# Kernel tuning notes

Hardware: AMD Instinct MI355X
Metric: run time of the kernel (lower is better)

The kernel has to match this reference:

```python
import jax, jax.numpy as jnp
import numpy as np

N_HEADS = 4
DIM_HEAD = 32


def setup_inputs() -> dict:
    key = jax.random.key(0)
    k1, k2, k3, k4 = jax.random.split(key, 4)
    x = jax.random.normal(k1, (8, 64, 80, 1024), dtype=jnp.float32)
    # conv_qkv: 1x1 conv, no bias -> weight [3*heads*dim_head, dim_in_out]
    w_qkv = jax.random.normal(k2, (3 * N_HEADS * DIM_HEAD, 64), dtype=jnp.float32) * 0.05
    # conv_out: 1x1 conv with bias -> weight [dim_in_out, heads*dim_head], bias [dim_in_out]
    w_out = jax.random.normal(k3, (64, N_HEADS * DIM_HEAD), dtype=jnp.float32) * 0.05
    b_out = jax.random.normal(k4, (64,), dtype=jnp.float32) * 0.05
    return {"x": x, "w_qkv": w_qkv, "w_out": w_out, "b_out": b_out}


def reference(x, w_qkv, w_out, b_out):
    b, c, h, w = x.shape
    n = h * w
    # 1x1 conv == channel matmul
    qkv = jnp.einsum('bchw,oc->bohw', x, w_qkv)            # [b, 3*heads*dh, h, w]
    qkv = qkv.reshape(b, 3, N_HEADS, DIM_HEAD, n)          # qkv outermost, then heads, then c
    q, k, v = qkv[:, 0], qkv[:, 1], qkv[:, 2]              # each [b, heads, dh, n]
    k = jax.nn.softmax(k, axis=-1)                          # softmax over spatial positions
    context = jnp.einsum('bhdn,bhen->bhde', k, v)          # [b, heads, dh, dh]
    out = jnp.einsum('bhde,bhdn->bhen', context, q)        # [b, heads, dh, n]
    out = out.reshape(b, N_HEADS * DIM_HEAD, h, w)
    return jnp.einsum('bchw,oc->bohw', out, w_out) + b_out[None, :, None, None]
```

## Files before the change

kernel.cpp:

```cpp
#include <hip/hip_runtime.h>
#include <stdint.h>


#define N_POS 81920
#define NT    128
#define TILES 640

typedef short bf16x8 __attribute__((ext_vector_type(8)));
typedef float f32x4  __attribute__((ext_vector_type(4)));

__device__ __forceinline__ uint32_t packbf(float lo, float hi){
  uint32_t a = __float_as_uint(lo), b = __float_as_uint(hi);
  a = (a + 0x8000u) >> 16;
  b = (b + 0x8000u) & 0xffff0000u;
  return a | b;
}
__device__ __forceinline__ short bf16of(float v){
  return (short)((__float_as_uint(v) + 0x8000u) >> 16);
}

__global__ __launch_bounds__(512, 4) void kernA(
    const float* __restrict__ x, const float* __restrict__ w,
    float* __restrict__ pA, float* __restrict__ pZ, int nch, int tpc)
{
  __shared__ __align__(16) uint16_t xs_cp[64 * 136];
  __shared__ __align__(16) uint16_t xs_pc[128 * 72];
  __shared__ __align__(16) uint16_t es[128 * 136];

  const int t  = threadIdx.x;
  const int w8 = t >> 6;
  const int l  = t & 63;
  const int lm = l & 15;
  const int lg = l >> 4;

  const int b  = blockIdx.x / nch;
  const int ch = blockIdx.x % nch;
  const float* xb = x + (size_t)b * 64 * N_POS;

  const int rr  = t >> 3;
  const int pg  = t & 7;
  const int spp = t & 127;
  const int scg = t >> 7;

  const int pth = w8 & 3;
  const int ht0 = (w8 >> 2) * 4;

  bf16x8 wkf[4][2];
  #pragma unroll
  for (int i = 0; i < 4; ++i)
    #pragma unroll
    for (int kk = 0; kk < 2; ++kk){
      const float* wp = w + (size_t)(128 + 16*(ht0+i) + lm) * 64 + 32*kk + 8*lg;
      float4 w0 = *(const float4*)wp;
      float4 w1 = *(const float4*)(wp + 4);
      bf16x8 f;
      f[0]=bf16of(w0.x); f[1]=bf16of(w0.y); f[2]=bf16of(w0.z); f[3]=bf16of(w0.w);
      f[4]=bf16of(w1.x); f[5]=bf16of(w1.y); f[6]=bf16of(w1.z); f[7]=bf16of(w1.w);
      wkf[i][kk] = f;
    }

  bf16x8 ones;
  #pragma unroll
  for (int j = 0; j < 8; ++j) ones[j] = (short)0x3F80;

  f32x4 acc[4], zac;
  zac = (f32x4){0.f,0.f,0.f,0.f};
  #pragma unroll
  for (int n = 0; n < 4; ++n) acc[n] = (f32x4){0.f,0.f,0.f,0.f};

  float4 fa0, fa1, fa2, fa3;
  float v[16];
  {
    const int n0 = (ch * tpc) * NT;
    const float* ga = xb + (size_t)rr * N_POS + n0 + 16*pg;
    fa0 = *(const float4*)ga;       fa1 = *(const float4*)(ga + 4);
    fa2 = *(const float4*)(ga + 8); fa3 = *(const float4*)(ga + 12);
    const float* gb = xb + (size_t)(16*scg) * N_POS + n0 + spp;
    #pragma unroll
    for (int i = 0; i < 16; ++i) v[i] = gb[(size_t)i * N_POS];
  }

  for (int tile = 0; tile < tpc; ++tile){
    __syncthreads();
    {
      uint4 u0, u1;
      u0.x = packbf(fa0.x,fa0.y); u0.y = packbf(fa0.z,fa0.w);
      u0.z = packbf(fa1.x,fa1.y); u0.w = packbf(fa1.z,fa1.w);
      u1.x = packbf(fa2.x,fa2.y); u1.y = packbf(fa2.z,fa2.w);
      u1.z = packbf(fa3.x,fa3.y); u1.w = packbf(fa3.z,fa3.w);
      *(uint4*)&xs_cp[rr*136 + 16*pg]     = u0;
      *(uint4*)&xs_cp[rr*136 + 16*pg + 8] = u1;
      uint4 p0, p1;
      p0.x = packbf(v[0],v[1]);   p0.y = packbf(v[2],v[3]);
      p0.z = packbf(v[4],v[5]);   p0.w = packbf(v[6],v[7]);
      p1.x = packbf(v[8],v[9]);   p1.y = packbf(v[10],v[11]);
      p1.z = packbf(v[12],v[13]); p1.w = packbf(v[14],v[15]);
      *(uint4*)&xs_pc[spp*72 + 16*scg]     = p0;
      *(uint4*)&xs_pc[spp*72 + 16*scg + 8] = p1;
    }
    __syncthreads();
    if (tile + 1 < tpc){
      const int n1 = (ch * tpc + tile + 1) * NT;
      const float* ga = xb + (size_t)rr * N_POS + n1 + 16*pg;
      fa0 = *(const float4*)ga;       fa1 = *(const float4*)(ga + 4);
      fa2 = *(const float4*)(ga + 8); fa3 = *(const float4*)(ga + 12);
      const float* gb = xb + (size_t)(16*scg) * N_POS + n1 + spp;
      #pragma unroll
      for (int i = 0; i < 16; ++i) v[i] = gb[(size_t)i * N_POS];
    }
    #pragma unroll
    for (int ip = 0; ip < 2; ++ip){
      const int pt = pth + 4*ip;
      bf16x8 af0 = *(const bf16x8*)&xs_pc[(16*pt + lm)*72 + 8*lg];
      bf16x8 af1 = *(const bf16x8*)&xs_pc[(16*pt + lm)*72 + 32 + 8*lg];
      #pragma unroll
      for (int i = 0; i < 4; ++i){
        f32x4 s = (f32x4){0.f,0.f,0.f,0.f};
        s = __builtin_amdgcn_mfma_f32_16x16x32_bf16(af0, wkf[i][0], s, 0,0,0);
        s = __builtin_amdgcn_mfma_f32_16x16x32_bf16(af1, wkf[i][1], s, 0,0,0);
        float e0 = __expf(s[0]), e1 = __expf(s[1]);
        float e2 = __expf(s[2]), e3 = __expf(s[3]);
        uint2 pk; pk.x = packbf(e0,e1); pk.y = packbf(e2,e3);
        *(uint2*)&es[(16*(ht0+i) + lm)*136 + 16*pt + 4*lg] = pk;
      }
    }
    __syncthreads();
    __builtin_amdgcn_s_setprio(1);
    #pragma unroll
    for (int kk = 0; kk < 4; ++kk){
      bf16x8 ea = *(const bf16x8*)&es[(16*w8 + lm)*136 + 32*kk + 8*lg];
      bf16x8 xbf[4];
      #pragma unroll
      for (int n = 0; n < 4; ++n)
        xbf[n] = *(const bf16x8*)&xs_cp[(16*n + lm)*136 + 32*kk + 8*lg];
      #pragma unroll
      for (int n = 0; n < 4; ++n)
        acc[n] = __builtin_amdgcn_mfma_f32_16x16x32_bf16(ea, xbf[n], acc[n], 0,0,0);
      zac = __builtin_amdgcn_mfma_f32_16x16x32_bf16(ea, ones, zac, 0,0,0);
    }
    __builtin_amdgcn_s_setprio(0);
  }

  float* pa = pA + (size_t)blockIdx.x * 8192;
  const int hd0 = 16*w8 + 4*lg;
  #pragma unroll
  for (int n = 0; n < 4; ++n)
    #pragma unroll
    for (int r = 0; r < 4; ++r)
      pa[(size_t)(hd0 + r)*64 + 16*n + lm] = acc[n][r];
  if (lm == 0){
    #pragma unroll
    for (int r = 0; r < 4; ++r)
      pZ[(size_t)blockIdx.x * 128 + hd0 + r] = zac[r];
  }
}

__global__ __launch_bounds__(256) void kernR1(
    const float* __restrict__ pA, const float* __restrict__ pZ,
    float* __restrict__ Ar, float* __restrict__ Zr, int nch)
{
  const int b = blockIdx.x >> 3, s = blockIdx.x & 7;
  const int off = s * 1024 + threadIdx.x * 4;
  float4 a = make_float4(0.f, 0.f, 0.f, 0.f);
  for (int ch = 0; ch < nch; ++ch){
    float4 v = *(const float4*)&pA[(size_t)(b * nch + ch) * 8192 + off];
    a.x += v.x; a.y += v.y; a.z += v.z; a.w += v.w;
  }
  *(float4*)&Ar[(size_t)b * 8192 + off] = a;
  if (s == 0 && threadIdx.x < 128){
    float z = 0.f;
    for (int ch = 0; ch < nch; ++ch) z += pZ[(size_t)(b * nch + ch) * 128 + threadIdx.x];
    Zr[b * 128 + threadIdx.x] = z;
  }
}

__global__ __launch_bounds__(256) void kernCM(
    const float* __restrict__ Ar, const float* __restrict__ Zr,
    const float* __restrict__ w_qkv, const float* __restrict__ w_out,
    float* __restrict__ M)
{
  __shared__ float A[128 * 65];
  __shared__ float Z[128];
  __shared__ float cs[128 * 33];
  __shared__ float T[64 * 129];
  const int b = blockIdx.x, t = threadIdx.x;

  #pragma unroll
  for (int k = 0; k < 32; ++k){
    int i = t + 256 * k;
    A[(i >> 6) * 65 + (i & 63)] = Ar[(size_t)b * 8192 + i];
  }
  if (t < 128) Z[t] = Zr[b * 128 + t];
  __syncthreads();

  {
    const int hd = t & 127, h = hd >> 5, e0 = (t >> 7) * 16;
    const float rz = 1.0f / Z[hd];
    for (int je = 0; je < 16; ++je){
      int e = e0 + je;
      const float* wv = w_qkv + (size_t)(256 + 32 * h + e) * 64;
      float a = 0.f;
      #pragma unroll
      for (int c = 0; c < 64; ++c) a = fmaf(A[hd * 65 + c], wv[c], a);
      cs[hd * 33 + e] = a * rz;
    }
  }
  __syncthreads();

  const int o = t & 63, g = t >> 6;
  for (int jh = 0; jh < 32; ++jh){
    int hd = 32 * g + jh;
    const float* wo = w_out + (size_t)o * 128 + 32 * g;
    float a = 0.f;
    #pragma unroll
    for (int e = 0; e < 32; ++e) a = fmaf(wo[e], cs[hd * 33 + e], a);
    T[o * 129 + hd] = a;
  }
  __syncthreads();

  const int c0 = 16 * g;
  float m[16];
  #pragma unroll
  for (int j = 0; j < 16; ++j) m[j] = 0.f;
  for (int hd = 0; hd < 128; ++hd){
    float tv = T[o * 129 + hd];
    const float* wq = w_qkv + (size_t)hd * 64 + c0;
    #pragma unroll
    for (int j = 0; j < 16; ++j) m[j] = fmaf(tv, wq[j], m[j]);
  }
  #pragma unroll
  for (int j = 0; j < 16; ++j) M[(size_t)b * 4096 + o * 64 + c0 + j] = m[j];
}

__global__ __launch_bounds__(256, 4) void kernO(
    const float* __restrict__ x, const float* __restrict__ M,
    const float* __restrict__ b_out, float* __restrict__ out)
{
  __shared__ __align__(16) uint16_t xs[256 * 72];

  const int t  = threadIdx.x;
  const int wv = t >> 6;
  const int l  = t & 63;
  const int lm = l & 15;
  const int lg = l >> 4;

  const int b  = blockIdx.x / 320;
  const int p0 = (blockIdx.x % 320) * 256;
  const float* xb = x + (size_t)b * 64 * N_POS + p0;

  const float* Mb = M + (size_t)b * 4096;
  bf16x8 mb[4][2];
  float bias[4];
  #pragma unroll
  for (int ot = 0; ot < 4; ++ot){
    bias[ot] = b_out[16*ot + lm];
    #pragma unroll
    for (int kk = 0; kk < 2; ++kk){
      const float* mp = Mb + (size_t)(16*ot + lm)*64 + 32*kk + 8*lg;
      float4 m0 = *(const float4*)mp;
      float4 m1 = *(const float4*)(mp + 4);
      bf16x8 f;
      f[0]=bf16of(m0.x); f[1]=bf16of(m0.y); f[2]=bf16of(m0.z); f[3]=bf16of(m0.w);
      f[4]=bf16of(m1.x); f[5]=bf16of(m1.y); f[6]=bf16of(m1.z); f[7]=bf16of(m1.w);
      mb[ot][kk] = f;
    }
  }

  #pragma unroll
  for (int cc = 0; cc < 8; ++cc){
    float v[8];
    #pragma unroll
    for (int j = 0; j < 8; ++j)
      v[j] = xb[(size_t)(8*cc + j) * N_POS + t];
    uint4 u;
    u.x = packbf(v[0],v[1]); u.y = packbf(v[2],v[3]);
    u.z = packbf(v[4],v[5]); u.w = packbf(v[6],v[7]);
    *(uint4*)&xs[t*72 + 8*cc] = u;
  }
  __syncthreads();

  float* ob = out + (size_t)b * 64 * N_POS + p0;

  #pragma unroll
  for (int ip = 0; ip < 4; ++ip){
    const int pt = 4*wv + ip;
    bf16x8 af0 = *(const bf16x8*)&xs[(16*pt + lm)*72 + 8*lg];
    bf16x8 af1 = *(const bf16x8*)&xs[(16*pt + lm)*72 + 32 + 8*lg];
    #pragma unroll
    for (int ot = 0; ot < 4; ++ot){
      f32x4 d = (f32x4){0.f,0.f,0.f,0.f};
      d = __builtin_amdgcn_mfma_f32_16x16x32_bf16(af0, mb[ot][0], d, 0,0,0);
      d = __builtin_amdgcn_mfma_f32_16x16x32_bf16(af1, mb[ot][1], d, 0,0,0);
      float4 st = make_float4(d[0]+bias[ot], d[1]+bias[ot],
                              d[2]+bias[ot], d[3]+bias[ot]);
      *(float4*)&ob[(size_t)(16*ot + lm) * N_POS + 16*pt + 4*lg] = st;
    }
  }
}

extern "C" void kernel_launch(void* const* d_in, const int* in_sizes, int n_in,
                              void* d_out, int out_size, void* d_ws, size_t ws_size,
                              hipStream_t stream)
{
  const float* x     = (const float*)d_in[0];
  const float* w_qkv = (const float*)d_in[1];
  const float* w_out = (const float*)d_in[2];
  const float* b_out = (const float*)d_in[3];
  float* out = (float*)d_out;
  float* ws  = (float*)d_ws;

  static const int cand[] = {64, 40, 32, 20, 16, 10, 8, 5, 4, 2, 1};
  int nch = 1;
  for (int i = 0; i < 11; ++i){
    size_t need = ((size_t)8 * cand[i] * (8192 + 128)
                   + 8 * 8192 + 8 * 128 + (size_t)8 * 4096) * 4;
    if (need <= ws_size){ nch = cand[i]; break; }
  }
  const int tpc = TILES / nch;

  float* pA  = ws;
  float* pZ  = pA + (size_t)8 * nch * 8192;
  float* Ar  = pZ + (size_t)8 * nch * 128;
  float* Zr  = Ar + (size_t)8 * 8192;
  float* M   = Zr + (size_t)8 * 128;

  kernA<<<8 * nch, 512, 0, stream>>>(x, w_qkv, pA, pZ, nch, tpc);
  kernR1<<<64,     256, 0, stream>>>(pA, pZ, Ar, Zr, nch);
  kernCM<<<8,      256, 0, stream>>>(Ar, Zr, w_qkv, w_out, M);
  kernO<<<2560,    256, 0, stream>>>(x, M, b_out, out);
}
```

Measured before the change: 204.0 us.

## Make output kernel persistent over five tiles with double-buffered LDS prefetch

```diff
diff --git a/kernel.cpp b/kernel.cpp
--- a/kernel.cpp
+++ b/kernel.cpp
@@ -232,11 +232,11 @@
   for (int j = 0; j < 16; ++j) M[(size_t)b * 4096 + o * 64 + c0 + j] = m[j];
 }
 
-__global__ __launch_bounds__(256, 4) void kernO(
+__global__ __launch_bounds__(256, 2) void kernO(
     const float* __restrict__ x, const float* __restrict__ M,
     const float* __restrict__ b_out, float* __restrict__ out)
 {
-  __shared__ __align__(16) uint16_t xs[256 * 72];
+  __shared__ __align__(16) uint16_t xs[2][256 * 72];
 
   const int t  = threadIdx.x;
   const int wv = t >> 6;
@@ -244,9 +244,10 @@
   const int lm = l & 15;
   const int lg = l >> 4;
 
-  const int b  = blockIdx.x / 320;
-  const int p0 = (blockIdx.x % 320) * 256;
-  const float* xb = x + (size_t)b * 64 * N_POS + p0;
+  const int b  = blockIdx.x >> 6;
+  const int tg = blockIdx.x & 63;
+  const float* xb = x   + (size_t)b * 64 * N_POS + tg * 1280;
+  float*       ob = out + (size_t)b * 64 * N_POS + tg * 1280;
 
   const float* Mb = M + (size_t)b * 4096;
   bf16x8 mb[4][2];
@@ -266,34 +267,57 @@
     }
   }
 
+  uint4 st[8];
+
   #pragma unroll
   for (int cc = 0; cc < 8; ++cc){
     float v[8];
     #pragma unroll
     for (int j = 0; j < 8; ++j)
       v[j] = xb[(size_t)(8*cc + j) * N_POS + t];
-    uint4 u;
-    u.x = packbf(v[0],v[1]); u.y = packbf(v[2],v[3]);
-    u.z = packbf(v[4],v[5]); u.w = packbf(v[6],v[7]);
-    *(uint4*)&xs[t*72 + 8*cc] = u;
-  }
+    st[cc].x = packbf(v[0],v[1]); st[cc].y = packbf(v[2],v[3]);
+    st[cc].z = packbf(v[4],v[5]); st[cc].w = packbf(v[6],v[7]);
+  }
+  #pragma unroll
+  for (int cc = 0; cc < 8; ++cc)
+    *(uint4*)&xs[0][t*72 + 8*cc] = st[cc];
   __syncthreads();
 
-  float* ob = out + (size_t)b * 64 * N_POS + p0;
-
-  #pragma unroll
-  for (int ip = 0; ip < 4; ++ip){
-    const int pt = 4*wv + ip;
-    bf16x8 af0 = *(const bf16x8*)&xs[(16*pt + lm)*72 + 8*lg];
-    bf16x8 af1 = *(const bf16x8*)&xs[(16*pt + lm)*72 + 32 + 8*lg];
-    #pragma unroll
-    for (int ot = 0; ot < 4; ++ot){
-      f32x4 d = (f32x4){0.f,0.f,0.f,0.f};
-      d = __builtin_amdgcn_mfma_f32_16x16x32_bf16(af0, mb[ot][0], d, 0,0,0);
-      d = __builtin_amdgcn_mfma_f32_16x16x32_bf16(af1, mb[ot][1], d, 0,0,0);
-      float4 st = make_float4(d[0]+bias[ot], d[1]+bias[ot],
-                              d[2]+bias[ot], d[3]+bias[ot]);
-      *(float4*)&ob[(size_t)(16*ot + lm) * N_POS + 16*pt + 4*lg] = st;
+  for (int tile = 0; tile < 5; ++tile){
+    const int cur = tile & 1;
+    if (tile < 4){
+      const float* gn = xb + (tile + 1) * 256 + t;
+      #pragma unroll
+      for (int cc = 0; cc < 8; ++cc){
+        float v[8];
+        #pragma unroll
+        for (int j = 0; j < 8; ++j)
+          v[j] = gn[(size_t)(8*cc + j) * N_POS];
+        st[cc].x = packbf(v[0],v[1]); st[cc].y = packbf(v[2],v[3]);
+        st[cc].z = packbf(v[4],v[5]); st[cc].w = packbf(v[6],v[7]);
+      }
+    }
+    const int pp0 = tile * 256;
+    #pragma unroll
+    for (int ip = 0; ip < 4; ++ip){
+      const int pt = 4*wv + ip;
+      bf16x8 af0 = *(const bf16x8*)&xs[cur][(16*pt + lm)*72 + 8*lg];
+      bf16x8 af1 = *(const bf16x8*)&xs[cur][(16*pt + lm)*72 + 32 + 8*lg];
+      #pragma unroll
+      for (int ot = 0; ot < 4; ++ot){
+        f32x4 d = (f32x4){0.f,0.f,0.f,0.f};
+        d = __builtin_amdgcn_mfma_f32_16x16x32_bf16(af0, mb[ot][0], d, 0,0,0);
+        d = __builtin_amdgcn_mfma_f32_16x16x32_bf16(af1, mb[ot][1], d, 0,0,0);
+        float4 stv = make_float4(d[0]+bias[ot], d[1]+bias[ot],
+                                 d[2]+bias[ot], d[3]+bias[ot]);
+        *(float4*)&ob[(size_t)(16*ot + lm) * N_POS + pp0 + 16*pt + 4*lg] = stv;
+      }
+    }
+    if (tile < 4){
+      #pragma unroll
+      for (int cc = 0; cc < 8; ++cc)
+        *(uint4*)&xs[cur ^ 1][t*72 + 8*cc] = st[cc];
+      __syncthreads();
     }
   }
 }
@@ -327,5 +351,5 @@
   kernA<<<8 * nch, 512, 0, stream>>>(x, w_qkv, pA, pZ, nch, tpc);
   kernR1<<<64,     256, 0, stream>>>(pA, pZ, Ar, Zr, nch);
   kernCM<<<8,      256, 0, stream>>>(Ar, Zr, w_qkv, w_out, M);
-  kernO<<<2560,    256, 0, stream>>>(x, M, b_out, out);
-}
+  kernO<<<512,     256, 0, stream>>>(x, M, b_out, out);
+}
```

Measured after the change: 209.4 us. 2.6% more time.
